# Performance work log

Measured on AMD Instinct MI355X. Metric: run time of the kernel, lower is better.

Reference implementation:

```python
import jax, jax.numpy as jnp
import numpy as np

B, T, I = 32, 512, 96
H, M, R, K = 256, 6, 16, 16
TASK, SENS = 32, 64
MPG = M // 3  # mechanisms per group
OUT = 64


def setup_inputs() -> dict:
    key = jax.random.key(0)
    ks = jax.random.split(key, 12)
    inp = {
        'x': jax.random.normal(ks[0], (B, T, I), jnp.float32),
        # stacked per-mechanism LowRankRNNCell params
        'W_ip': jax.random.normal(ks[1], (M, H, H), jnp.float32) / np.sqrt(H),
        'b_ip': jnp.zeros((M, H), jnp.float32),
        'U': jax.random.normal(ks[2], (M, H, R), jnp.float32) / np.sqrt(R),
        'Vr': jax.random.normal(ks[3], (M, R, H), jnp.float32) / np.sqrt(H),
        'cell_bias': jnp.zeros((M, H), jnp.float32),
        'W_in_task': 0.01 * jax.random.normal(ks[4], (MPG, TASK, H), jnp.float32),
        'W_in_sensory': 0.01 * jax.random.normal(ks[5], (MPG, SENS, H), jnp.float32),
        'W_Q': 0.01 * jax.random.normal(ks[6], (M, H, K), jnp.float32),
        'W_K': 0.01 * jax.random.normal(ks[7], (M, H, K), jnp.float32),
        'W_V': 0.01 * jax.random.normal(ks[8], (M, H, H), jnp.float32),
        'W_out': jax.random.normal(ks[9], (H * MPG, OUT), jnp.float32) / np.sqrt(H * MPG),
        'b_out': jnp.zeros((OUT,), jnp.float32),
    }
    return inp


def _rim_forward(x, W_ip, b_ip, U, Vr, cell_bias, W_in_task, W_in_sensory,
                 W_Q, W_K, W_V, W_out, b_out):
    scale = jnp.float32(1.0 / np.sqrt(K))

    def step(Hs, x_t):
        # input routing: group 0 <- task input, group 1 <- sensory, group 2 <- zeros
        x_task = x_t[:, -TASK:]
        x_sens = x_t[:, :-TASK]
        g0 = jnp.einsum('bi,mih->bmh', x_task, W_in_task)
        g1 = jnp.einsum('bi,mih->bmh', x_sens, W_in_sensory)
        A_in = jnp.concatenate([g0, g1, jnp.zeros_like(g0)], axis=1)  # [B,M,H]
        # batched LowRankRNNCell update per mechanism
        inp_part = jnp.einsum('bmi,mih->bmh', A_in, W_ip) + b_ip
        rec = jnp.einsum('bmr,mrh->bmh', jnp.einsum('bmh,mhr->bmr', Hs, U), Vr)
        H_in = jnp.tanh(inp_part + rec + cell_bias)  # [B,M,H]
        # communication attention (exact einsum structure of the original)
        Qc = jnp.einsum('bmh,mhk->bmk', H_in, W_Q)
        Kc = jnp.einsum('bmh,mhk->bmk', H_in, W_K)
        Vc = jnp.einsum('bmh,mhj->bjm', H_in, W_V)  # V_comm[b,h,m]
        attn = jax.nn.softmax(jnp.einsum('bmk,bnk->bmn', Qc, Kc) * scale, axis=-1)
        A_comm = jnp.einsum('bmn,bhm->bnh', attn, Vc)
        H_new = H_in + A_comm
        out = H_new[:, -MPG:].reshape(H_new.shape[0], -1) @ W_out + b_out
        return H_new, (out, H_new, A_in, A_comm, attn)

    H0 = jnp.zeros((x.shape[0], M, H), x.dtype)
    _, (outs, Hseq, Ain_seq, Acomm_seq, attn_seq) = jax.lax.scan(
        step, H0, jnp.swapaxes(x, 0, 1))
    # time-major -> batch-major where the torch code stacks on dim=1 (outputs)
    outputs = jnp.swapaxes(outs, 0, 1)  # [B,T,OUT]
    return outputs, Hseq, Ain_seq, Acomm_seq, attn_seq


def reference(x, W_ip, b_ip, U, Vr, cell_bias, W_in_task, W_in_sensory,
              W_Q, W_K, W_V, W_out, b_out):
    return _rim_forward(x, W_ip, b_ip, U, Vr, cell_bias, W_in_task,
                        W_in_sensory, W_Q, W_K, W_V, W_out, b_out)
```

## Files before the change

kernel.cpp:

```cpp
#include <hip/hip_runtime.h>
#include <math.h>

#define BB 32
#define TT 512
#define II 96
#define HH 256
#define MM 6
#define RR 16
#define KK 16
#define OUTD 64

#define O_HSEQ  1048576
#define O_AIN   26214400
#define O_ACM   51380224
#define O_ATTN  76546048

#define WS_WEFF 0
#define WS_UT   49152
#define WS_WQT  73728
#define WS_WKT  98304
#define WS_VC   122880
#define WS_QG   221184
#define WS_KG   227328
#define WS_FLAG 233472
#define WS_COOP_FLOATS 233984

__global__ __launch_bounds__(256) void rim_weff(
    const float* __restrict__ Wtask, const float* __restrict__ Wsens,
    const float* __restrict__ Wip,
    const float* __restrict__ U, const float* __restrict__ WQ, const float* __restrict__ WK,
    float* __restrict__ Weff, float* __restrict__ Ut, float* __restrict__ WQt, float* __restrict__ WKt)
{
  __shared__ float row[256];
  const int bidx = blockIdx.x;
  const int tid = threadIdx.x;
  if (bidx < 192) {
    int m, i;
    if (bidx < 32)       { m = 0; i = bidx; }
    else if (bidx < 64)  { m = 1; i = bidx - 32; }
    else if (bidx < 128) { m = 2; i = bidx - 64; }
    else                 { m = 3; i = bidx - 128; }
    row[tid] = (m < 2) ? Wtask[(m * 32 + i) * 256 + tid]
                       : Wsens[((m - 2) * 64 + i) * 256 + tid];
    __syncthreads();
    float acc = 0.f;
    const float* wip = Wip + m * 65536 + tid;
    #pragma unroll 8
    for (int j = 0; j < 256; ++j) acc += row[j] * wip[j * 256];
    const int base = (m == 0) ? 0 : (m == 1) ? 8192 : (m == 2) ? 16384 : 32768;
    Weff[base + i * 256 + tid] = acc;
  } else {
    const int p = bidx - 192;
    const int m = p >> 4, r = p & 15;
    Ut [(m * 16 + r) * 256 + tid] = U [m * 4096 + tid * 16 + r];
    WQt[(m * 16 + r) * 256 + tid] = WQ[m * 4096 + tid * 16 + r];
    WKt[(m * 16 + r) * 256 + tid] = WK[m * 4096 + tid * 16 + r];
  }
}

__global__ __launch_bounds__(256) void rim_pre(
    const float* __restrict__ x,
    const float* __restrict__ Wtask, const float* __restrict__ Wsens,
    float* __restrict__ Ain)
{
  __shared__ float xr[16][96];
  const int tid = threadIdx.x;
  const int rb0 = blockIdx.x * 16;
  for (int idx = tid; idx < 16 * 96; idx += 256) {
    int r = idx / 96, c = idx % 96;
    int rb = rb0 + r; int t = rb >> 5, b = rb & 31;
    xr[r][c] = x[(b * TT + t) * II + c];
  }
  __syncthreads();
  const int h = tid;
  float acc[16];

  for (int m = 0; m < 4; ++m) {
    const int cnt  = (m < 2) ? 32 : 64;
    const int xoff = (m < 2) ? 64 : 0;
    const float* W = (m < 2) ? (Wtask + m * 32 * 256) : (Wsens + (m - 2) * 64 * 256);
    #pragma unroll
    for (int r = 0; r < 16; ++r) acc[r] = 0.f;
    for (int i = 0; i < cnt; ++i) {
      float w = W[i * 256 + h];
      #pragma unroll
      for (int r = 0; r < 16; ++r) acc[r] += xr[r][xoff + i] * w;
    }
    #pragma unroll
    for (int r = 0; r < 16; ++r) {
      int rb = rb0 + r; int t = rb >> 5, b = rb & 31;
      Ain[((t * 32 + b) * 6 + m) * 256 + h] = acc[r];
    }
  }
  #pragma unroll
  for (int r = 0; r < 16; ++r) {
    int rb = rb0 + r; int t = rb >> 5, b = rb & 31;
    Ain[((t * 32 + b) * 6 + 4) * 256 + h] = 0.f;
    Ain[((t * 32 + b) * 6 + 5) * 256 + h] = 0.f;
  }
}

__global__ __launch_bounds__(512, 2) void rim_step(
    const float* __restrict__ x,
    const float* __restrict__ Vr, const float* __restrict__ WV,
    const float* __restrict__ bip, const float* __restrict__ cbias,
    const float* __restrict__ UtW, const float* __restrict__ WQtW,
    const float* __restrict__ WKtW, const float* __restrict__ WeffW,
    float* __restrict__ VcG, float* __restrict__ QG, float* __restrict__ KG,
    unsigned int* __restrict__ flags,
    float* __restrict__ Hseq, float* __restrict__ Acm, float* __restrict__ attnO)
{
  __shared__ __align__(16) float Hl[256];
  __shared__ __align__(16) float Hin[256];
  __shared__ float biasl[256];
  __shared__ float Utl[16][256];
  __shared__ float Vrl[16][256];
  __shared__ float WQtl[16][256];
  __shared__ float WKtl[16][256];
  __shared__ float Weffl[64][256];
  __shared__ float Vcp[2][256];
  __shared__ float tmpUr[16];
  __shared__ float Qcl[16], Kcl[16];
  __shared__ float attnl[40];
  __shared__ float xl[96];
  __shared__ float qkl[192];

  const int bid = blockIdx.x;
  const int m = bid >> 5;
  const int b = bid & 31;
  const int tid = threadIdx.x;
  const int wid = tid >> 5, lane = tid & 31;
  const int h_out = tid & 255, p = tid >> 8;

  const int base = (m == 0) ? 0 : (m == 1) ? 8192 : (m == 2) ? 16384 : 32768;
  const int cnt  = (m < 2) ? 32 : 64;
  const int xoff = (m < 2) ? 64 : 0;

  for (int i = tid; i < 4096; i += 512) {
    ((float*)Utl)[i]  = UtW [m * 4096 + i];
    ((float*)Vrl)[i]  = Vr  [m * 4096 + i];
    ((float*)WQtl)[i] = WQtW[m * 4096 + i];
    ((float*)WKtl)[i] = WKtW[m * 4096 + i];
  }
  if (m < 4)
    for (int i = tid; i < cnt * 256; i += 512)
      ((float*)Weffl)[i] = WeffW[base + i];
  if (tid < 256) {
    biasl[tid] = bip[m * 256 + tid] + cbias[m * 256 + tid];
    Hl[tid] = 0.f;
  }
  float w[128];
  #pragma unroll
  for (int j = 0; j < 128; ++j)
    w[j] = WV[((size_t)(m * 256 + p * 128 + j)) * 256 + h_out];
  __syncthreads();

  for (int t = 0; t < TT; ++t) {
    const int buf = t & 1;
    const int xbase = (buf * 32 + b);

    if (m < 4 && tid < 96) xl[tid] = x[(b * TT + t) * II + tid];

    {
      const float* up = &Utl[wid][0];
      float s = 0.f;
      #pragma unroll
      for (int h = lane; h < 256; h += 32) s += Hl[h] * up[h];
      #pragma unroll
      for (int off = 16; off > 0; off >>= 1) s += __shfl_down(s, off, 32);
      if (lane == 0) tmpUr[wid] = s;
    }
    __syncthreads();

    if (tid < 256) {
      float rec = 0.f;
      #pragma unroll
      for (int r = 0; r < 16; ++r) rec += tmpUr[r] * Vrl[r][tid];
      float inp = 0.f;
      if (m < 4)
        for (int i = 0; i < cnt; ++i) inp += xl[xoff + i] * Weffl[i][tid];
      Hin[tid] = tanhf(inp + rec + biasl[tid]);
    }
    __syncthreads();

    {
      float acc = 0.f;
      const float4* h4 = (const float4*)&Hin[p * 128];
      #pragma unroll
      for (int q = 0; q < 32; ++q) {
        float4 hv = h4[q];
        acc += hv.x * w[4 * q] + hv.y * w[4 * q + 1]
             + hv.z * w[4 * q + 2] + hv.w * w[4 * q + 3];
      }
      Vcp[p][h_out] = acc;
    }
    {
      const int g = tid >> 4, l = tid & 15;
      const int r = g & 15;
      const float* wp = (g < 16) ? &WQtl[r][0] : &WKtl[r][0];
      float s = 0.f;
      #pragma unroll
      for (int j = 0; j < 16; ++j) { int h = l + 16 * j; s += Hin[h] * wp[h]; }
      s += __shfl_down(s, 8, 16);
      s += __shfl_down(s, 4, 16);
      s += __shfl_down(s, 2, 16);
      s += __shfl_down(s, 1, 16);
      if (l == 0) { if (g < 16) Qcl[r] = s; else Kcl[r] = s; }
    }
    __syncthreads();

    if (tid < 256)
      __hip_atomic_store(&VcG[(xbase * 6 + m) * 256 + tid],
                         Vcp[0][tid] + Vcp[1][tid],
                         __ATOMIC_RELAXED, __HIP_MEMORY_SCOPE_SYSTEM);
    if (tid < 16)
      __hip_atomic_store(&QG[(xbase * 6 + m) * 16 + tid], Qcl[tid],
                         __ATOMIC_RELAXED, __HIP_MEMORY_SCOPE_SYSTEM);
    else if (tid < 32)
      __hip_atomic_store(&KG[(xbase * 6 + m) * 16 + tid - 16], Kcl[tid - 16],
                         __ATOMIC_RELAXED, __HIP_MEMORY_SCOPE_SYSTEM);
    asm volatile("s_waitcnt vmcnt(0)" ::: "memory");
    __syncthreads();

    if (tid == 0) {
      __hip_atomic_fetch_add(&flags[b * 16], 1u,
                             __ATOMIC_RELAXED, __HIP_MEMORY_SCOPE_SYSTEM);
      const unsigned target = 6u * (unsigned)(t + 1);
      while (__hip_atomic_load(&flags[b * 16],
                               __ATOMIC_RELAXED, __HIP_MEMORY_SCOPE_SYSTEM) < target) { }
    }
    __syncthreads();

    float vcv[6];
    if (tid < 256) {
      #pragma unroll
      for (int mm = 0; mm < 6; ++mm)
        vcv[mm] = __hip_atomic_load(&VcG[(xbase * 6 + mm) * 256 + tid],
                                    __ATOMIC_RELAXED, __HIP_MEMORY_SCOPE_SYSTEM);
    }
    if (tid < 96)
      qkl[tid] = __hip_atomic_load(&QG[xbase * 96 + tid],
                                   __ATOMIC_RELAXED, __HIP_MEMORY_SCOPE_SYSTEM);
    else if (tid < 192)
      qkl[tid] = __hip_atomic_load(&KG[xbase * 96 + tid - 96],
                                   __ATOMIC_RELAXED, __HIP_MEMORY_SCOPE_SYSTEM);
    __syncthreads();

    if (tid < 6) {
      float sc[6]; float mx = -1e30f;
      #pragma unroll
      for (int n = 0; n < 6; ++n) {
        float s = 0.f;
        #pragma unroll
        for (int k = 0; k < 16; ++k) s += qkl[tid * 16 + k] * qkl[96 + n * 16 + k];
        sc[n] = s * 0.25f;
        mx = fmaxf(mx, sc[n]);
      }
      float sm = 0.f;
      #pragma unroll
      for (int n = 0; n < 6; ++n) { sc[n] = expf(sc[n] - mx); sm += sc[n]; }
      float inv = 1.f / sm;
      #pragma unroll
      for (int n = 0; n < 6; ++n) attnl[tid * 6 + n] = sc[n] * inv;
    }
    __syncthreads();
    if (m == 0 && tid < 36) attnO[(size_t)(t * 32 + b) * 36 + tid] = attnl[tid];

    if (tid < 256) {
      float ac = 0.f;
      #pragma unroll
      for (int mm = 0; mm < 6; ++mm) ac += attnl[mm * 6 + m] * vcv[mm];
      float hn = Hin[tid] + ac;
      Hl[tid] = hn;
      size_t gi = ((size_t)(t * 32 + b) * 6 + m) * 256 + tid;
      Hseq[gi] = hn;
      Acm[gi]  = ac;
    }
    __syncthreads();
  }
}

__global__ __launch_bounds__(256) void rim_out(
    const float* __restrict__ Hseq, const float* __restrict__ Wout,
    const float* __restrict__ bout, float* __restrict__ out0)
{
  __shared__ float hrow[4][512];
  const int tid = threadIdx.x;
  const int row0 = blockIdx.x * 4;
  for (int i = tid; i < 4 * 512; i += 256) {
    int r = i >> 9, j = i & 511;
    int rb = row0 + r; int b = rb >> 9, t = rb & 511;
    hrow[r][j] = Hseq[((size_t)(t * 32 + b) * 6 + 4 + (j >> 8)) * 256 + (j & 255)];
  }
  __syncthreads();
  const int r = tid >> 6, o = tid & 63;
  const int rb = row0 + r;
  float s = bout[o];
  const float* hp = hrow[r];
  const float* wp = Wout + o;
  #pragma unroll 8
  for (int j = 0; j < 512; ++j) s += hp[j] * wp[(size_t)j * 64];
  out0[(size_t)rb * 64 + o] = s;
}

__global__ __launch_bounds__(512) void rim_loop(
    const float* __restrict__ x,
    const float* __restrict__ Vr, const float* __restrict__ WV,
    const float* __restrict__ Wout, const float* __restrict__ bout,
    const float* __restrict__ bip, const float* __restrict__ cbias,
    const float* __restrict__ Ut, const float* __restrict__ WQt, const float* __restrict__ WKt,
    const float* __restrict__ Weff,
    float* __restrict__ out0, float* __restrict__ Hseq,
    float* __restrict__ Acm, float* __restrict__ attnO)
{
  __shared__ float Hl[6][256];
  __shared__ float Hin[6][256];
  __shared__ float biasl[6][256];
  __shared__ float Vcp[2][6][256];
  __shared__ float tmpUr[6][16];
  __shared__ float Qc[6][16], Kc[6][16];
  __shared__ float attnl[36];
  __shared__ float pout[8][64];
  __shared__ float xl[96];
  __shared__ float inpl[4][256];

  const int b = blockIdx.x;
  const int tid = threadIdx.x;
  const int wid = tid >> 5, lane = tid & 31;

  for (int i = tid; i < 1536; i += 512) {
    int m = i >> 8, h = i & 255;
    biasl[m][h] = bip[i] + cbias[i];
    Hl[m][h] = 0.f;
  }
  __syncthreads();

  for (int t = 0; t < TT; ++t) {
    if (tid < 96) xl[tid] = x[(b * TT + t) * II + tid];
    __syncthreads();
    for (int mh = tid; mh < 1024; mh += 512) {
      int m = mh >> 8, h = mh & 255;
      const int base = (m == 0) ? 0 : (m == 1) ? 8192 : (m == 2) ? 16384 : 32768;
      const int cnt  = (m < 2) ? 32 : 64;
      const int xoff = (m < 2) ? 64 : 0;
      float a = 0.f;
      for (int i = 0; i < cnt; ++i) a += xl[xoff + i] * Weff[base + i * 256 + h];
      inpl[m][h] = a;
    }

    for (int pq = wid; pq < 96; pq += 16) {
      int m = pq >> 4, r = pq & 15;
      const float* up = Ut + (m * 16 + r) * 256;
      float s = 0.f;
      #pragma unroll
      for (int h = lane; h < 256; h += 32) s += Hl[m][h] * up[h];
      #pragma unroll
      for (int off = 16; off > 0; off >>= 1) s += __shfl_down(s, off, 32);
      if (lane == 0) tmpUr[m][r] = s;
    }
    __syncthreads();

    for (int mh = tid; mh < 1536; mh += 512) {
      int m = mh >> 8, h = mh & 255;
      float rec = 0.f;
      const float* vp = Vr + m * 4096 + h;
      #pragma unroll
      for (int r = 0; r < 16; ++r) rec += tmpUr[m][r] * vp[r * 256];
      float pre = (m < 4) ? inpl[m][h] : 0.f;
      Hin[m][h] = tanhf(pre + rec + biasl[m][h]);
    }
    __syncthreads();

    for (int pq = wid; pq < 192; pq += 16) {
      int q = pq % 96;
      int m = q >> 4, k = q & 15;
      const float* wp = ((pq < 96) ? WQt : WKt) + (m * 16 + k) * 256;
      float s = 0.f;
      #pragma unroll
      for (int h = lane; h < 256; h += 32) s += Hin[m][h] * wp[h];
      #pragma unroll
      for (int off = 16; off > 0; off >>= 1) s += __shfl_down(s, off, 32);
      if (lane == 0) { if (pq < 96) Qc[m][k] = s; else Kc[m][k] = s; }
    }

    {
      const int h_out = tid & 255, half = tid >> 8;
      for (int m = 0; m < 6; ++m) {
        const float* wv = WV + ((size_t)(m * 256 + half * 128)) * 256 + h_out;
        const float* hv = &Hin[m][half * 128];
        float s = 0.f;
        #pragma unroll 8
        for (int j = 0; j < 128; ++j) s += hv[j] * wv[(size_t)j * 256];
        Vcp[half][m][h_out] = s;
      }
    }
    __syncthreads();

    if (tid < 36) {
      int m = tid / 6, n = tid % 6;
      float s = 0.f;
      #pragma unroll
      for (int k = 0; k < 16; ++k) s += Qc[m][k] * Kc[n][k];
      attnl[tid] = s * 0.25f;
    }
    __syncthreads();
    if (tid < 6) {
      int m = tid;
      float mx = -1e30f;
      #pragma unroll
      for (int n = 0; n < 6; ++n) mx = fmaxf(mx, attnl[m * 6 + n]);
      float e[6], sm = 0.f;
      #pragma unroll
      for (int n = 0; n < 6; ++n) { e[n] = expf(attnl[m * 6 + n] - mx); sm += e[n]; }
      float inv = 1.f / sm;
      #pragma unroll
      for (int n = 0; n < 6; ++n) attnl[m * 6 + n] = e[n] * inv;
    }
    __syncthreads();
    if (tid < 36) attnO[(size_t)(t * 32 + b) * 36 + tid] = attnl[tid];

    for (int mh = tid; mh < 1536; mh += 512) {
      int n = mh >> 8, h = mh & 255;
      float ac = 0.f;
      #pragma unroll
      for (int m = 0; m < 6; ++m)
        ac += attnl[m * 6 + n] * (Vcp[0][m][h] + Vcp[1][m][h]);
      float hn = Hin[n][h] + ac;
      Hl[n][h] = hn;
      size_t gi = ((size_t)(t * 32 + b) * 6 + n) * 256 + h;
      Hseq[gi] = hn;
      Acm[gi]  = ac;
    }
    __syncthreads();

    {
      const int o = tid & 63, js = tid >> 6;
      const float* hp = &Hl[4][0];
      const float* wp = Wout + (size_t)(js * 64) * 64 + o;
      float s = 0.f;
      #pragma unroll 8
      for (int jj = 0; jj < 64; ++jj) s += hp[js * 64 + jj] * wp[(size_t)jj * 64];
      pout[js][o] = s;
    }
    __syncthreads();
    if (tid < 64) {
      float s = bout[tid];
      #pragma unroll
      for (int js = 0; js < 8; ++js) s += pout[js][tid];
      out0[(size_t)(b * TT + t) * 64 + tid] = s;
    }
  }
}

extern "C" void kernel_launch(void* const* d_in, const int* in_sizes, int n_in,
                              void* d_out, int out_size, void* d_ws, size_t ws_size,
                              hipStream_t stream) {
  const float* x    = (const float*)d_in[0];
  const float* W_ip = (const float*)d_in[1];
  const float* b_ip = (const float*)d_in[2];
  const float* U    = (const float*)d_in[3];
  const float* Vr   = (const float*)d_in[4];
  const float* cb   = (const float*)d_in[5];
  const float* Wt   = (const float*)d_in[6];
  const float* Wsn  = (const float*)d_in[7];
  const float* WQ   = (const float*)d_in[8];
  const float* WK   = (const float*)d_in[9];
  const float* WV   = (const float*)d_in[10];
  const float* Wo   = (const float*)d_in[11];
  const float* bo   = (const float*)d_in[12];

  float* out  = (float*)d_out;
  float* Hseq = out + O_HSEQ;
  float* Ain  = out + O_AIN;
  float* Acm  = out + O_ACM;
  float* attn = out + O_ATTN;

  float* ws   = (float*)d_ws;
  float* Weff = ws + WS_WEFF;
  float* Ut   = ws + WS_UT;
  float* WQt  = ws + WS_WQT;
  float* WKt  = ws + WS_WKT;

  hipLaunchKernelGGL(rim_weff, dim3(288), dim3(256), 0, stream,
                     Wt, Wsn, W_ip, U, WQ, WK, Weff, Ut, WQt, WKt);
  hipLaunchKernelGGL(rim_pre, dim3(1024), dim3(256), 0, stream,
                     x, Wt, Wsn, Ain);

  if (ws_size >= (size_t)WS_COOP_FLOATS * sizeof(float)) {
    float* VcG = ws + WS_VC;
    float* QG  = ws + WS_QG;
    float* KG  = ws + WS_KG;
    unsigned int* flags = (unsigned int*)(ws + WS_FLAG);
    hipMemsetAsync((void*)flags, 0, 512 * sizeof(unsigned int), stream);

    void* args[] = { (void*)&x, (void*)&Vr, (void*)&WV, (void*)&b_ip, (void*)&cb,
                     (void*)&Ut, (void*)&WQt, (void*)&WKt, (void*)&Weff,
                     (void*)&VcG, (void*)&QG, (void*)&KG, (void*)&flags,
                     (void*)&Hseq, (void*)&Acm, (void*)&attn };
    hipLaunchCooperativeKernel((void*)rim_step, dim3(192), dim3(512), args, 0, stream);

    hipLaunchKernelGGL(rim_out, dim3(4096), dim3(256), 0, stream,
                       Hseq, Wo, bo, out);
  } else {
    hipLaunchKernelGGL(rim_loop, dim3(32), dim3(512), 0, stream,
                       x, Vr, WV, Wo, bo, b_ip, cb, Ut, WQt, WKt, Weff,
                       out, Hseq, Acm, attn);
  }
}
```

Measured before the change: 3.004 ms.

## Specialize wavefronts in recurrent step and split cross-block barrier into per-mechanism flags

The per-timestep block-wide fetch-add barrier is replaced by per-mechanism sequence flags. One wave publishes Q/K and signals, another waits only for Q/K and computes the softmax, and the Vc-ready wait is deferred until just before the attention mix. The input projection for the next step is precomputed by spare waves from a double-buffered prefetched x, the full W_V column is held in registers by 256 threads, and LDS rows are padded and some barriers lightened. This shortens the serial critical path per timestep, but raises register pressure (256 floats per thread, occupancy 1) and makes the flag protocol more complex.

Result: slower. 5.525 ms (+83.9%).

```diff
diff --git a/kernel.cpp b/kernel.cpp
--- a/kernel.cpp
+++ b/kernel.cpp
@@ -6,8 +6,6 @@
 #define II 96
 #define HH 256
 #define MM 6
-#define RR 16
-#define KK 16
 #define OUTD 64
 
 #define O_HSEQ  1048576
@@ -20,10 +18,11 @@
 #define WS_WQT  73728
 #define WS_WKT  98304
 #define WS_VC   122880
-#define WS_QG   221184
-#define WS_KG   227328
+#define WS_QK   221184
 #define WS_FLAG 233472
 #define WS_COOP_FLOATS 233984
+
+#define LBAR() asm volatile("s_waitcnt lgkmcnt(0)\n\ts_barrier" ::: "memory")
 
 __global__ __launch_bounds__(256) void rim_weff(
     const float* __restrict__ Wtask, const float* __restrict__ Wsens,
@@ -100,47 +99,47 @@
   }
 }
 
-__global__ __launch_bounds__(512, 2) void rim_step(
+__global__ __launch_bounds__(512, 1) void rim_step(
     const float* __restrict__ x,
     const float* __restrict__ Vr, const float* __restrict__ WV,
     const float* __restrict__ bip, const float* __restrict__ cbias,
     const float* __restrict__ UtW, const float* __restrict__ WQtW,
     const float* __restrict__ WKtW, const float* __restrict__ WeffW,
-    float* __restrict__ VcG, float* __restrict__ QG, float* __restrict__ KG,
-    unsigned int* __restrict__ flags,
+    float* __restrict__ VcG, float* __restrict__ QKG,
+    unsigned int* __restrict__ seqG,
     float* __restrict__ Hseq, float* __restrict__ Acm, float* __restrict__ attnO)
 {
   __shared__ __align__(16) float Hl[256];
   __shared__ __align__(16) float Hin[256];
   __shared__ float biasl[256];
-  __shared__ float Utl[16][256];
-  __shared__ float Vrl[16][256];
-  __shared__ float WQtl[16][256];
-  __shared__ float WKtl[16][256];
+  __shared__ float Utl[16][257];
+  __shared__ float Vrl[16][257];
+  __shared__ float WQtl[16][257];
+  __shared__ float WKtl[16][257];
   __shared__ float Weffl[64][256];
-  __shared__ float Vcp[2][256];
+  __shared__ float inpl[2][256];
+  __shared__ float xl[2][96];
   __shared__ float tmpUr[16];
-  __shared__ float Qcl[16], Kcl[16];
   __shared__ float attnl[40];
-  __shared__ float xl[96];
   __shared__ float qkl[192];
 
   const int bid = blockIdx.x;
   const int m = bid >> 5;
   const int b = bid & 31;
   const int tid = threadIdx.x;
-  const int wid = tid >> 5, lane = tid & 31;
-  const int h_out = tid & 255, p = tid >> 8;
+  const int w64 = tid >> 6, lane = tid & 63;
+  const int g32 = tid >> 5, l32 = tid & 31;
 
   const int base = (m == 0) ? 0 : (m == 1) ? 8192 : (m == 2) ? 16384 : 32768;
   const int cnt  = (m < 2) ? 32 : 64;
   const int xoff = (m < 2) ? 64 : 0;
 
   for (int i = tid; i < 4096; i += 512) {
-    ((float*)Utl)[i]  = UtW [m * 4096 + i];
-    ((float*)Vrl)[i]  = Vr  [m * 4096 + i];
-    ((float*)WQtl)[i] = WQtW[m * 4096 + i];
-    ((float*)WKtl)[i] = WKtW[m * 4096 + i];
+    int r = i >> 8, c = i & 255;
+    Utl [r][c] = UtW [m * 4096 + i];
+    Vrl [r][c] = Vr  [m * 4096 + i];
+    WQtl[r][c] = WQtW[m * 4096 + i];
+    WKtl[r][c] = WKtW[m * 4096 + i];
   }
   if (m < 4)
     for (int i = tid; i < cnt * 256; i += 512)
@@ -149,134 +148,152 @@
     biasl[tid] = bip[m * 256 + tid] + cbias[m * 256 + tid];
     Hl[tid] = 0.f;
   }
-  float w[128];
-  #pragma unroll
-  for (int j = 0; j < 128; ++j)
-    w[j] = WV[((size_t)(m * 256 + p * 128 + j)) * 256 + h_out];
+  float xreg = 0.f;
+  if (m < 4 && tid < 96) {
+    xl[0][tid] = x[((size_t)b * TT + 0) * II + tid];
+    xreg       = x[((size_t)b * TT + 1) * II + tid];
+  }
+  float w[256];
+  if (tid < 256) {
+    #pragma unroll
+    for (int j = 0; j < 256; ++j)
+      w[j] = WV[((size_t)(m * 256 + j)) * 256 + tid];
+  }
+  __syncthreads();
+  if (m < 4 && tid < 256) {
+    float a = 0.f;
+    for (int i = 0; i < cnt; ++i) a += xl[0][xoff + i] * Weffl[i][tid];
+    inpl[0][tid] = a;
+  }
   __syncthreads();
 
   for (int t = 0; t < TT; ++t) {
     const int buf = t & 1;
-    const int xbase = (buf * 32 + b);
-
-    if (m < 4 && tid < 96) xl[tid] = x[(b * TT + t) * II + tid];
+    const int xb6 = (buf * 32 + b) * 6;
+
+    if (m < 4 && tid < 96) {
+      xl[(t + 1) & 1][tid] = xreg;
+      xreg = (t + 2 < TT) ? x[((size_t)b * TT + t + 2) * II + tid] : 0.f;
+    }
 
     {
-      const float* up = &Utl[wid][0];
       float s = 0.f;
-      #pragma unroll
-      for (int h = lane; h < 256; h += 32) s += Hl[h] * up[h];
+      const float* up = &Utl[g32][0];
+      #pragma unroll
+      for (int h = l32; h < 256; h += 32) s += Hl[h] * up[h];
       #pragma unroll
       for (int off = 16; off > 0; off >>= 1) s += __shfl_down(s, off, 32);
-      if (lane == 0) tmpUr[wid] = s;
-    }
-    __syncthreads();
+      if (l32 == 0) tmpUr[g32] = s;
+    }
+    LBAR();
 
     if (tid < 256) {
       float rec = 0.f;
       #pragma unroll
       for (int r = 0; r < 16; ++r) rec += tmpUr[r] * Vrl[r][tid];
-      float inp = 0.f;
-      if (m < 4)
-        for (int i = 0; i < cnt; ++i) inp += xl[xoff + i] * Weffl[i][tid];
+      float inp = (m < 4) ? inpl[buf][tid] : 0.f;
       Hin[tid] = tanhf(inp + rec + biasl[tid]);
     }
-    __syncthreads();
-
-    {
-      float acc = 0.f;
-      const float4* h4 = (const float4*)&Hin[p * 128];
-      #pragma unroll
-      for (int q = 0; q < 32; ++q) {
+    LBAR();
+
+    float acc = 0.f;
+    if (w64 < 4) {
+      const float4* h4 = (const float4*)Hin;
+      #pragma unroll
+      for (int q = 0; q < 64; ++q) {
         float4 hv = h4[q];
         acc += hv.x * w[4 * q] + hv.y * w[4 * q + 1]
              + hv.z * w[4 * q + 2] + hv.w * w[4 * q + 3];
       }
-      Vcp[p][h_out] = acc;
-    }
-    {
-      const int g = tid >> 4, l = tid & 15;
-      const int r = g & 15;
-      const float* wp = (g < 16) ? &WQtl[r][0] : &WKtl[r][0];
+      __hip_atomic_store(&VcG[(xb6 + m) * 256 + tid], acc,
+                         __ATOMIC_RELAXED, __HIP_MEMORY_SCOPE_SYSTEM);
+    } else if (w64 == 4) {
+      const int o = lane >> 1, hf = lane & 1, h0 = hf * 128;
+      const float* wp = (o < 16) ? &WQtl[o][0] : &WKtl[o - 16][0];
       float s = 0.f;
       #pragma unroll
-      for (int j = 0; j < 16; ++j) { int h = l + 16 * j; s += Hin[h] * wp[h]; }
-      s += __shfl_down(s, 8, 16);
-      s += __shfl_down(s, 4, 16);
-      s += __shfl_down(s, 2, 16);
-      s += __shfl_down(s, 1, 16);
-      if (l == 0) { if (g < 16) Qcl[r] = s; else Kcl[r] = s; }
-    }
-    __syncthreads();
-
-    if (tid < 256)
-      __hip_atomic_store(&VcG[(xbase * 6 + m) * 256 + tid],
-                         Vcp[0][tid] + Vcp[1][tid],
+      for (int j = 0; j < 128; ++j) s += Hin[h0 + j] * wp[h0 + j];
+      s += __shfl_down(s, 1, 64);
+      if (hf == 0)
+        __hip_atomic_store(&QKG[(buf * 32 + b) * 192 + m * 32 + o], s,
+                           __ATOMIC_RELAXED, __HIP_MEMORY_SCOPE_SYSTEM);
+      asm volatile("s_waitcnt vmcnt(0)" ::: "memory");
+      if (lane == 0)
+        __hip_atomic_store(&seqG[b * 16 + m], (unsigned)(t + 1),
+                           __ATOMIC_RELAXED, __HIP_MEMORY_SCOPE_SYSTEM);
+    } else if (w64 == 7) {
+      if (lane < 6) {
+        while (__hip_atomic_load(&seqG[b * 16 + lane],
+                                 __ATOMIC_RELAXED, __HIP_MEMORY_SCOPE_SYSTEM)
+               < (unsigned)(t + 1)) {}
+      }
+      const int qb = (buf * 32 + b) * 192;
+      float q0 = __hip_atomic_load(&QKG[qb + lane],       __ATOMIC_RELAXED, __HIP_MEMORY_SCOPE_SYSTEM);
+      float q1 = __hip_atomic_load(&QKG[qb + 64 + lane],  __ATOMIC_RELAXED, __HIP_MEMORY_SCOPE_SYSTEM);
+      float q2 = __hip_atomic_load(&QKG[qb + 128 + lane], __ATOMIC_RELAXED, __HIP_MEMORY_SCOPE_SYSTEM);
+      qkl[lane] = q0; qkl[64 + lane] = q1; qkl[128 + lane] = q2;
+    } else {
+      if (m < 4) {
+        const int h0 = (tid - 320) * 2;
+        const int nb = (t + 1) & 1;
+        float a0 = 0.f, a1 = 0.f;
+        for (int i = 0; i < cnt; ++i) {
+          float xv = xl[nb][xoff + i];
+          a0 += xv * Weffl[i][h0];
+          a1 += xv * Weffl[i][h0 + 1];
+        }
+        inpl[nb][h0] = a0; inpl[nb][h0 + 1] = a1;
+      }
+    }
+    __syncthreads();
+
+    if (tid == 0)
+      __hip_atomic_store(&seqG[b * 16 + 8 + m], (unsigned)(t + 1),
                          __ATOMIC_RELAXED, __HIP_MEMORY_SCOPE_SYSTEM);
-    if (tid < 16)
-      __hip_atomic_store(&QG[(xbase * 6 + m) * 16 + tid], Qcl[tid],
-                         __ATOMIC_RELAXED, __HIP_MEMORY_SCOPE_SYSTEM);
-    else if (tid < 32)
-      __hip_atomic_store(&KG[(xbase * 6 + m) * 16 + tid - 16], Kcl[tid - 16],
-                         __ATOMIC_RELAXED, __HIP_MEMORY_SCOPE_SYSTEM);
-    asm volatile("s_waitcnt vmcnt(0)" ::: "memory");
-    __syncthreads();
-
-    if (tid == 0) {
-      __hip_atomic_fetch_add(&flags[b * 16], 1u,
-                             __ATOMIC_RELAXED, __HIP_MEMORY_SCOPE_SYSTEM);
-      const unsigned target = 6u * (unsigned)(t + 1);
-      while (__hip_atomic_load(&flags[b * 16],
-                               __ATOMIC_RELAXED, __HIP_MEMORY_SCOPE_SYSTEM) < target) { }
-    }
-    __syncthreads();
-
-    float vcv[6];
-    if (tid < 256) {
-      #pragma unroll
-      for (int mm = 0; mm < 6; ++mm)
-        vcv[mm] = __hip_atomic_load(&VcG[(xbase * 6 + mm) * 256 + tid],
-                                    __ATOMIC_RELAXED, __HIP_MEMORY_SCOPE_SYSTEM);
-    }
-    if (tid < 96)
-      qkl[tid] = __hip_atomic_load(&QG[xbase * 96 + tid],
-                                   __ATOMIC_RELAXED, __HIP_MEMORY_SCOPE_SYSTEM);
-    else if (tid < 192)
-      qkl[tid] = __hip_atomic_load(&KG[xbase * 96 + tid - 96],
-                                   __ATOMIC_RELAXED, __HIP_MEMORY_SCOPE_SYSTEM);
-    __syncthreads();
-
-    if (tid < 6) {
+    if (w64 == 7 && lane < 6) {
       float sc[6]; float mx = -1e30f;
       #pragma unroll
       for (int n = 0; n < 6; ++n) {
         float s = 0.f;
         #pragma unroll
-        for (int k = 0; k < 16; ++k) s += qkl[tid * 16 + k] * qkl[96 + n * 16 + k];
-        sc[n] = s * 0.25f;
-        mx = fmaxf(mx, sc[n]);
+        for (int k = 0; k < 16; ++k) s += qkl[lane * 32 + k] * qkl[n * 32 + 16 + k];
+        sc[n] = s * 0.25f; mx = fmaxf(mx, sc[n]);
       }
       float sm = 0.f;
       #pragma unroll
       for (int n = 0; n < 6; ++n) { sc[n] = expf(sc[n] - mx); sm += sc[n]; }
       float inv = 1.f / sm;
       #pragma unroll
-      for (int n = 0; n < 6; ++n) attnl[tid * 6 + n] = sc[n] * inv;
-    }
-    __syncthreads();
-    if (m == 0 && tid < 36) attnO[(size_t)(t * 32 + b) * 36 + tid] = attnl[tid];
+      for (int n = 0; n < 6; ++n) {
+        float a = sc[n] * inv;
+        attnl[lane * 6 + n] = a;
+        if (m == 0) attnO[((size_t)t * 32 + b) * 36 + lane * 6 + n] = a;
+      }
+    }
+    if (w64 == 0 && lane < 6) {
+      while (__hip_atomic_load(&seqG[b * 16 + 8 + lane],
+                               __ATOMIC_RELAXED, __HIP_MEMORY_SCOPE_SYSTEM)
+             < (unsigned)(t + 1)) {}
+    }
+    LBAR();
 
     if (tid < 256) {
+      float vcv[6];
+      #pragma unroll
+      for (int mm = 0; mm < 6; ++mm)
+        vcv[mm] = (mm == m) ? acc
+                 : __hip_atomic_load(&VcG[(xb6 + mm) * 256 + tid],
+                                     __ATOMIC_RELAXED, __HIP_MEMORY_SCOPE_SYSTEM);
       float ac = 0.f;
       #pragma unroll
       for (int mm = 0; mm < 6; ++mm) ac += attnl[mm * 6 + m] * vcv[mm];
       float hn = Hin[tid] + ac;
       Hl[tid] = hn;
-      size_t gi = ((size_t)(t * 32 + b) * 6 + m) * 256 + tid;
+      size_t gi = (((size_t)t * 32 + b) * 6 + m) * 256 + tid;
       Hseq[gi] = hn;
       Acm[gi]  = ac;
     }
-    __syncthreads();
+    LBAR();
   }
 }
 
@@ -488,14 +505,13 @@
 
   if (ws_size >= (size_t)WS_COOP_FLOATS * sizeof(float)) {
     float* VcG = ws + WS_VC;
-    float* QG  = ws + WS_QG;
-    float* KG  = ws + WS_KG;
-    unsigned int* flags = (unsigned int*)(ws + WS_FLAG);
-    hipMemsetAsync((void*)flags, 0, 512 * sizeof(unsigned int), stream);
+    float* QKG = ws + WS_QK;
+    unsigned int* seqG = (unsigned int*)(ws + WS_FLAG);
+    hipMemsetAsync((void*)seqG, 0, 512 * sizeof(unsigned int), stream);
 
     void* args[] = { (void*)&x, (void*)&Vr, (void*)&WV, (void*)&b_ip, (void*)&cb,
                      (void*)&Ut, (void*)&WQt, (void*)&WKt, (void*)&Weff,
-                     (void*)&VcG, (void*)&QG, (void*)&KG, (void*)&flags,
+                     (void*)&VcG, (void*)&QKG, (void*)&seqG,
                      (void*)&Hseq, (void*)&Acm, (void*)&attn };
     hipLaunchCooperativeKernel((void*)rim_step, dim3(192), dim3(512), args, 0, stream);
 
```
